# Kernel optimization log

Measured on AMD Instinct MI355X. Metric: run time of the kernel, lower is better.

The kernel has to match this reference:

```python
import jax, jax.numpy as jnp
import numpy as np

N = 50000   # num entities
R2 = 480    # num_rels * 2
D = 200     # h_dim
T = 4       # sequence_len (graph snapshots)
E = 100000  # edges per snapshot
L = 2       # rgcn layers
SLOPE = (1.0 / 8.0 + 1.0 / 3.0) / 2.0  # deterministic rrelu (eval-mode expected slope)


def setup_inputs() -> dict:
    key = jax.random.key(0)
    ks = jax.random.split(key, 13)
    s = 1.0 / np.sqrt(D)
    w = lambda k, shp, sc: jax.random.normal(k, shp, dtype=jnp.float32) * sc
    return {
        "src": jax.random.randint(ks[0], (T, E), 0, N, dtype=jnp.int32),
        "dst": jax.random.randint(ks[1], (T, E), 0, N, dtype=jnp.int32),
        "etype": jax.random.randint(ks[2], (T, E), 0, R2, dtype=jnp.int32),
        "dynamic_emb": w(ks[3], (N, D), 1.0),
        "emb_rel": w(ks[4], (R2, D), s),
        "W_ih": w(ks[5], (3 * D, 2 * D), s),
        "W_hh": w(ks[6], (3 * D, D), s),
        "b_ih": jnp.zeros((3 * D,), jnp.float32),
        "b_hh": jnp.zeros((3 * D,), jnp.float32),
        "W_neighbor": w(ks[7], (L, D, D), s),
        "W_loop": w(ks[8], (L, D, D), s),
        "time_gate_weight": w(ks[9], (D, D), s),
        "time_gate_bias": jnp.zeros((D,), jnp.float32),
    }


def _l2norm(x):
    n = jnp.linalg.norm(x, axis=-1, keepdims=True)
    return x / jnp.maximum(n, 1e-12)


def _gru(x, hprev, W_ih, W_hh, b_ih, b_hh):
    gi = x @ W_ih.T + b_ih
    gh = hprev @ W_hh.T + b_hh
    ir, iz, inn = jnp.split(gi, 3, axis=-1)
    hr, hz, hn = jnp.split(gh, 3, axis=-1)
    r = jax.nn.sigmoid(ir + hr)
    z = jax.nn.sigmoid(iz + hz)
    n = jnp.tanh(inn + r * hn)
    return (1.0 - z) * n + z * hprev


def reference(src, dst, etype, dynamic_emb, emb_rel, W_ih, W_hh, b_ih, b_hh,
              W_neighbor, W_loop, time_gate_weight, time_gate_bias):
    h_init = _l2norm(dynamic_emb)  # layer_norm=True path (F.normalize)

    def step(carry, g):
        h, h0 = carry
        s, d_, et = g
        # per-relation mean of entity embeddings touching that relation (r_to_e spans)
        ent_idx = jnp.concatenate([s, d_])          # [2E]
        seg = jnp.concatenate([et, et])             # [2E]
        ssum = jax.ops.segment_sum(h[ent_idx], seg, num_segments=R2)
        cnt = jax.ops.segment_sum(jnp.ones_like(seg, jnp.float32), seg, num_segments=R2)
        x_mean = ssum / jnp.maximum(cnt, 1.0)[:, None]          # absent rels stay 0
        x_input = jnp.concatenate([emb_rel, x_mean], axis=1)    # [R2, 2D]
        h0 = _l2norm(_gru(x_input, h0, W_ih, W_hh, b_ih, b_hh))
        # UnionRGCNLayer x L: gather -> sum-aggregate -> norm + self-loop -> rrelu
        deg = jax.ops.segment_sum(jnp.ones_like(d_, jnp.float32), d_, num_segments=N)
        norm = 1.0 / jnp.maximum(deg, 1.0)
        hh = h
        for l in range(L):
            pre = hh[s] + h0[et]                                  # [E, D]
            agg = jax.ops.segment_sum(pre, d_, num_segments=N) @ W_neighbor[l]
            out = agg * norm[:, None] + hh @ W_loop[l]
            hh = jnp.where(out >= 0, out, out * SLOPE)            # rrelu (eval)
        cur = _l2norm(hh)
        tw = jax.nn.sigmoid(h @ time_gate_weight + time_gate_bias)
        h = tw * cur + (1.0 - tw) * h
        return (h, h0), h

    (_, _), hist = jax.lax.scan(step, (h_init, emb_rel), (src, dst, etype))
    return hist  # [T, N, D] history of evolved entity embeddings
```

## Files before the change

### kernel.cpp

```cpp
#include <hip/hip_runtime.h>
#include <math.h>

#define NE 50000
#define R2C 480
#define DD 200
#define TT 4
#define EE 100000
#define SLOPE 0.22916666666666666f

#define SCCH 8
#define EPB (256 * SCCH)
#define APAD 224
#define WPAD 224
#define WSZ (208 * WPAD)
#define DCH 4096
#define DNC ((NE + DCH - 1) / DCH)

typedef short short8 __attribute__((ext_vector_type(8)));
typedef float float4v __attribute__((ext_vector_type(4)));

__device__ __forceinline__ float sigm(float x) { return 1.f / (1.f + expf(-x)); }

__device__ __forceinline__ short f2bf(float f) {
  union { float f; unsigned u; } v;
  v.f = f;
  unsigned r = v.u + 0x7fffu + ((v.u >> 16) & 1u);
  return (short)(r >> 16);
}


__global__ void init_h_kernel(const float* __restrict__ emb, float* __restrict__ h) {
  int n = blockIdx.x;
  int lane = threadIdx.x;
  size_t base = (size_t)n * DD;
  float v0 = emb[base + lane];
  float v1 = emb[base + 64 + lane];
  float v2 = emb[base + 128 + lane];
  float v3 = (lane < 8) ? emb[base + 192 + lane] : 0.f;
  float ss = v0 * v0 + v1 * v1 + v2 * v2 + v3 * v3;
#pragma unroll
  for (int off = 32; off; off >>= 1) ss += __shfl_down(ss, off);
  ss = __shfl(ss, 0);
  float inv = 1.f / fmaxf(sqrtf(ss), 1e-12f);
  h[base + lane] = v0 * inv;
  h[base + 64 + lane] = v1 * inv;
  h[base + 128 + lane] = v2 * inv;
  if (lane < 8) h[base + 192 + lane] = v3 * inv;
}

__global__ void copy_kernel(const float* __restrict__ a, float* __restrict__ b, int n) {
  int i = blockIdx.x * blockDim.x + threadIdx.x;
  if (i < n) b[i] = a[i];
}

__global__ void fill_x_kernel(const float* __restrict__ emb_rel, float* __restrict__ X) {
  int i = blockIdx.x * blockDim.x + threadIdx.x;
  if (i >= R2C * DD) return;
  int r = i / DD, d = i - r * DD;
  X[(size_t)r * 400 + d] = emb_rel[i];
}

__global__ void prep_w_kernel(const float* __restrict__ Wnb, const float* __restrict__ Wlp,
                              const float* __restrict__ Wtg, short* __restrict__ Wb) {
  int idx = blockIdx.x * 256 + threadIdx.x;
  if (idx >= 5 * WSZ) return;
  int m = idx / WSZ, rem = idx - m * WSZ;
  int n = rem / WPAD, k = rem - n * WPAD;
  const float* s;
  if (m == 0) s = Wnb;
  else if (m == 1) s = Wnb + DD * DD;
  else if (m == 2) s = Wlp;
  else if (m == 3) s = Wlp + DD * DD;
  else s = Wtg;
  float v = (n < DD && k < DD) ? s[(size_t)k * DD + n] : 0.f;
  Wb[idx] = f2bf(v);
}

__global__ __launch_bounds__(256) void hist_kernel(const int* __restrict__ et,
                                                   const int* __restrict__ dst,
                                                   int* __restrict__ et_hist,
                                                   int* __restrict__ deg_hist) {
  __shared__ int lh[R2C];
  int t = blockIdx.y;
  int tid = threadIdx.x;
  int e0 = blockIdx.x * EPB;
  for (int i = tid; i < R2C; i += 256) lh[i] = 0;
  __syncthreads();
#pragma unroll
  for (int c = 0; c < SCCH; c++) {
    int e = e0 + c * 256 + tid;
    if (e < EE) {
      atomicAdd(&lh[et[(size_t)t * EE + e]], 1);
      atomicAdd(&deg_hist[(size_t)t * NE + dst[(size_t)t * EE + e]], 1);
    }
  }
  __syncthreads();
  for (int i = tid; i < R2C; i += 256)
    if (lh[i]) atomicAdd(&et_hist[t * R2C + i], lh[i]);
}

__global__ void scan_rel_kernel(const int* __restrict__ et_hist, int* __restrict__ rowptr) {
  int t = blockIdx.x;
  int tid = threadIdx.x;
  __shared__ int s[512];
  int v = (tid < R2C) ? 2 * et_hist[t * R2C + tid] : 0;
  s[tid] = v;
  __syncthreads();
  for (int off = 1; off < 512; off <<= 1) {
    int x = (tid >= off) ? s[tid - off] : 0;
    __syncthreads();
    s[tid] += x;
    __syncthreads();
  }
  if (tid < R2C) rowptr[t * (R2C + 1) + tid] = s[tid] - v;
  if (tid == 0) rowptr[t * (R2C + 1) + R2C] = 2 * EE;
}

__global__ __launch_bounds__(256) void deg_partial_kernel(const int* __restrict__ deg_hist,
                                                          int* __restrict__ csum) {
  int t = blockIdx.y, c = blockIdx.x, tid = threadIdx.x;
  const int* dh = deg_hist + (size_t)t * NE;
  int base = c * DCH + tid * 16;
  int s = 0;
  if (base < NE) {
    int end = base + 16 > NE ? NE : base + 16;
    for (int i = base; i < end; i++) s += dh[i];
  }
  __shared__ int red[256];
  red[tid] = s;
  __syncthreads();
  for (int off = 128; off; off >>= 1) {
    if (tid < off) red[tid] += red[tid + off];
    __syncthreads();
  }
  if (tid == 0) csum[t * DNC + c] = red[0];
}

__global__ __launch_bounds__(256) void deg_emit_kernel(const int* __restrict__ deg_hist,
                                                       const int* __restrict__ csum,
                                                       int* __restrict__ rowptr,
                                                       float* __restrict__ normv) {
  int t = blockIdx.y, c = blockIdx.x, tid = threadIdx.x;
  const int* dh = deg_hist + (size_t)t * NE;
  __shared__ int scan[256];
  __shared__ int soff;
  int base = c * DCH + tid * 16;
  int s = 0;
  if (base < NE) {
    int end = base + 16 > NE ? NE : base + 16;
    for (int i = base; i < end; i++) s += dh[i];
  }
  scan[tid] = s;
  __syncthreads();
  for (int off = 1; off < 256; off <<= 1) {
    int x = (tid >= off) ? scan[tid - off] : 0;
    __syncthreads();
    scan[tid] += x;
    __syncthreads();
  }
  if (tid == 0) {
    int o = 0;
    for (int j = 0; j < c; j++) o += csum[t * DNC + j];
    soff = o;
  }
  __syncthreads();
  int run = soff + scan[tid] - s;
  if (base < NE) {
    int end = base + 16 > NE ? NE : base + 16;
    for (int i = base; i < end; i++) {
      int v = dh[i];
      rowptr[t * (NE + 1) + i] = run;
      normv[(size_t)t * NE + i] = 1.f / fmaxf((float)v, 1.f);
      run += v;
    }
  }
  if (c == 0 && tid == 0) rowptr[t * (NE + 1) + NE] = EE;
}

__global__ __launch_bounds__(256) void scatter_rel_kernel(const int* __restrict__ src,
                                                          const int* __restrict__ dst,
                                                          const int* __restrict__ et,
                                                          const int* __restrict__ rowptr,
                                                          int* __restrict__ cursor,
                                                          int* __restrict__ sorted_ent) {
  __shared__ int lcnt[R2C];
  __shared__ int lbase[R2C];
  int t = blockIdx.y;
  int tid = threadIdx.x;
  int e0 = blockIdx.x * EPB;
  for (int i = tid; i < R2C; i += 256) lcnt[i] = 0;
  __syncthreads();
  int rels[SCCH];
#pragma unroll
  for (int c = 0; c < SCCH; c++) {
    int e = e0 + c * 256 + tid;
    int r = (e < EE) ? et[(size_t)t * EE + e] : -1;
    rels[c] = r;
    if (r >= 0) atomicAdd(&lcnt[r], 2);
  }
  __syncthreads();
  const int* rp = rowptr + t * (R2C + 1);
  for (int i = tid; i < R2C; i += 256) {
    int c = lcnt[i];
    lbase[i] = rp[i] + (c ? atomicAdd(&cursor[t * R2C + i], c) : 0);
    lcnt[i] = 0;
  }
  __syncthreads();
  int* se = sorted_ent + (size_t)t * 2 * EE;
#pragma unroll
  for (int c = 0; c < SCCH; c++) {
    int r = rels[c];
    if (r >= 0) {
      int e = e0 + c * 256 + tid;
      int off = atomicAdd(&lcnt[r], 2);
      int p = lbase[r] + off;
      se[p] = src[(size_t)t * EE + e];
      se[p + 1] = dst[(size_t)t * EE + e];
    }
  }
}

__global__ void scatter_dst_kernel(const int* __restrict__ dst, const int* __restrict__ rowptr,
                                   int* __restrict__ cursor, int* __restrict__ sorted_edge) {
  int i = blockIdx.x * blockDim.x + threadIdx.x;
  if (i >= TT * EE) return;
  int t = i / EE, e = i - t * EE;
  int d = dst[i];
  int base = rowptr[t * (NE + 1) + d];
  int p = base + atomicAdd(&cursor[(size_t)t * NE + d], 1);
  sorted_edge[(size_t)t * EE + p] = e;
}


__global__ void relmean_part_kernel(const float* __restrict__ h, const int* __restrict__ rowptr,
                                    const int* __restrict__ sorted_ent_t,
                                    float* __restrict__ Xpart) {
  int r = blockIdx.x, j = blockIdx.y;
  int beg = rowptr[r], end = rowptr[r + 1];
  int lane = threadIdx.x & 63, w = threadIdx.x >> 6;
  float a0 = 0, a1 = 0, a2 = 0, a3 = 0;
  for (int i = beg + j * 4 + w; i < end; i += 16) {
    int idx = sorted_ent_t[i];
    const float* row = h + (size_t)idx * DD;
    a0 += row[lane];
    a1 += row[64 + lane];
    a2 += row[128 + lane];
    if (lane < 8) a3 += row[192 + lane];
  }
  __shared__ float part[4][DD];
  part[w][lane] = a0;
  part[w][64 + lane] = a1;
  part[w][128 + lane] = a2;
  if (lane < 8) part[w][192 + lane] = a3;
  __syncthreads();
  for (int d = threadIdx.x; d < DD; d += 256) {
    Xpart[((size_t)r * 4 + j) * DD + d] = part[0][d] + part[1][d] + part[2][d] + part[3][d];
  }
}

__global__ void relmean_comb_kernel(const float* __restrict__ Xpart,
                                    const int* __restrict__ rowptr, float* __restrict__ X) {
  int r = blockIdx.x;
  int d = threadIdx.x;
  if (d >= DD) return;
  float s = 0.f;
#pragma unroll
  for (int j = 0; j < 4; j++) s += Xpart[((size_t)r * 4 + j) * DD + d];
  float cnt = fmaxf((float)(rowptr[r + 1] - rowptr[r]), 1.f);
  X[(size_t)r * 400 + 200 + d] = s / cnt;
}

__global__ __launch_bounds__(256) void gemm_small_bt(const float* __restrict__ A,
                                                     const float* __restrict__ B,
                                                     float* __restrict__ C, int M, int N, int K) {
  __shared__ float As[16][33];
  __shared__ float Bs[16][33];
  int tid = threadIdx.x;
  int col0 = blockIdx.x * 32;
  int row0 = blockIdx.y * 32;
  int tr = tid >> 4, tc = tid & 15;
  float a00 = 0, a01 = 0, a10 = 0, a11 = 0;
  for (int k0 = 0; k0 < K; k0 += 16) {
    __syncthreads();
    for (int i = tid; i < 512; i += 256) {
      int kk = i & 15, r = i >> 4;
      int row = row0 + r, k = k0 + kk;
      As[kk][r] = (row < M && k < K) ? A[(size_t)row * K + k] : 0.f;
    }
    for (int i = tid; i < 512; i += 256) {
      int kk = i & 15, c = i >> 4;
      int col = col0 + c, k = k0 + kk;
      Bs[kk][c] = (col < N && k < K) ? B[(size_t)col * K + k] : 0.f;
    }
    __syncthreads();
#pragma unroll
    for (int kk = 0; kk < 16; kk++) {
      float x0 = As[kk][tr * 2], x1 = As[kk][tr * 2 + 1];
      float y0 = Bs[kk][tc * 2], y1 = Bs[kk][tc * 2 + 1];
      a00 += x0 * y0;
      a01 += x0 * y1;
      a10 += x1 * y0;
      a11 += x1 * y1;
    }
  }
  int row = row0 + tr * 2, col = col0 + tc * 2;
  if (row < M && col < N) C[(size_t)row * N + col] = a00;
  if (row < M && col + 1 < N) C[(size_t)row * N + col + 1] = a01;
  if (row + 1 < M && col < N) C[(size_t)(row + 1) * N + col] = a10;
  if (row + 1 < M && col + 1 < N) C[(size_t)(row + 1) * N + col + 1] = a11;
}

__global__ void gru_gate_kernel(const float* __restrict__ gi, const float* __restrict__ gh,
                                const float* __restrict__ b_ih, const float* __restrict__ b_hh,
                                float* __restrict__ h0) {
  int r = blockIdx.x;
  int tid = threadIdx.x;
  int lane = tid & 63, w = tid >> 6;
  __shared__ float red[4];
  float o = 0.f;
  if (tid < DD) {
    size_t b = (size_t)r * (3 * DD);
    float ir = gi[b + tid] + b_ih[tid];
    float iz = gi[b + DD + tid] + b_ih[DD + tid];
    float inn = gi[b + 2 * DD + tid] + b_ih[2 * DD + tid];
    float hr = gh[b + tid] + b_hh[tid];
    float hz = gh[b + DD + tid] + b_hh[DD + tid];
    float hn = gh[b + 2 * DD + tid] + b_hh[2 * DD + tid];
    float hv = h0[(size_t)r * DD + tid];
    float rr = sigm(ir + hr);
    float z = sigm(iz + hz);
    float n = tanhf(inn + rr * hn);
    o = (1.f - z) * n + z * hv;
  }
  float ss = o * o;
#pragma unroll
  for (int off = 32; off; off >>= 1) ss += __shfl_down(ss, off);
  if (lane == 0) red[w] = ss;
  __syncthreads();
  float tot = red[0] + red[1] + red[2] + red[3];
  float inv = 1.f / fmaxf(sqrtf(tot), 1e-12f);
  if (tid < DD) h0[(size_t)r * DD + tid] = o * inv;
}

__global__ void agg_kernel(const float* __restrict__ hh, const float* __restrict__ h0,
                           const int* __restrict__ rowptr, const int* __restrict__ sorted_edge_t,
                           const int* __restrict__ src_t, const int* __restrict__ et_t,
                           const float* __restrict__ normv_t, short* __restrict__ aggb) {
  int w = threadIdx.x >> 6, lane = threadIdx.x & 63;
  int n = blockIdx.x * 4 + w;
  if (n >= NE) return;
  int beg = rowptr[n], end = rowptr[n + 1];
  float a0 = 0, a1 = 0, a2 = 0, a3 = 0;
  for (int i = beg; i < end; i++) {
    int e = sorted_edge_t[i];
    const float* hr = hh + (size_t)src_t[e] * DD;
    const float* qr = h0 + (size_t)et_t[e] * DD;
    a0 += hr[lane] + qr[lane];
    a1 += hr[64 + lane] + qr[64 + lane];
    a2 += hr[128 + lane] + qr[128 + lane];
    if (lane < 8) a3 += hr[192 + lane] + qr[192 + lane];
  }
  float nm = normv_t[n];
  short* outp = aggb + (size_t)n * APAD;
  outp[lane] = f2bf(a0 * nm);
  outp[64 + lane] = f2bf(a1 * nm);
  outp[128 + lane] = f2bf(a2 * nm);
  if (lane < 8) outp[192 + lane] = f2bf(a3 * nm);
  else if (lane < 32) outp[192 + lane] = 0;
}


__global__ __launch_bounds__(256) void gemm_dual(const short* __restrict__ A1,
                                                 const short* __restrict__ Wb1,
                                                 const float* __restrict__ A2,
                                                 const short* __restrict__ Wb2,
                                                 float* __restrict__ C) {
  __shared__ short Bt[208][40];
  int tid = threadIdx.x;
  int lane = tid & 63, w = tid >> 6;
  int quad = lane >> 4, l16 = lane & 15;
  int row0 = blockIdx.x * 128;

  float4v acc[2][13];
#pragma unroll
  for (int rt = 0; rt < 2; rt++)
#pragma unroll
    for (int ct = 0; ct < 13; ct++) acc[rt][ct] = (float4v){0.f, 0.f, 0.f, 0.f};

  for (int pass = 0; pass < 2; ++pass) {
    const short* Wb = pass ? Wb2 : Wb1;
    for (int k0 = 0; k0 < DD; k0 += 32) {
      __syncthreads();
#pragma unroll
      for (int it = 0; it < 4; it++) {
        int c = tid + it * 256;
        if (c < 832) {
          int n = c % 208, k8 = (c / 208) * 8;
          *(short8*)&Bt[n][k8] = *(const short8*)&Wb[(size_t)n * WPAD + k0 + k8];
        }
      }
      __syncthreads();
      short8 af[2];
#pragma unroll
      for (int rt = 0; rt < 2; rt++) {
        int row = row0 + w * 32 + rt * 16 + l16;
        short8 a = (short8){0, 0, 0, 0, 0, 0, 0, 0};
        if (pass == 0) {
          if (row < NE) a = *(const short8*)(A1 + (size_t)row * APAD + k0 + quad * 8);
        } else {
          int kb = k0 + quad * 8;
          if (row < NE && kb < DD) {
            const float* ap = A2 + (size_t)row * DD + kb;
            float4v v0 = *(const float4v*)ap;
            float4v v1 = *(const float4v*)(ap + 4);
            short tmp[8] = {f2bf(v0[0]), f2bf(v0[1]), f2bf(v0[2]), f2bf(v0[3]),
                            f2bf(v1[0]), f2bf(v1[1]), f2bf(v1[2]), f2bf(v1[3])};
            a = *(short8*)&tmp[0];
          }
        }
        af[rt] = a;
      }
#pragma unroll
      for (int ct = 0; ct < 13; ct++) {
        short8 bf = *(short8*)&Bt[ct * 16 + l16][quad * 8];
        acc[0][ct] = __builtin_amdgcn_mfma_f32_16x16x32_bf16(af[0], bf, acc[0][ct], 0, 0, 0);
        acc[1][ct] = __builtin_amdgcn_mfma_f32_16x16x32_bf16(af[1], bf, acc[1][ct], 0, 0, 0);
      }
    }
  }
#pragma unroll
  for (int rt = 0; rt < 2; rt++) {
#pragma unroll
    for (int ct = 0; ct < 13; ct++) {
      int col = ct * 16 + l16;
      if (col >= DD) continue;
#pragma unroll
      for (int i = 0; i < 4; i++) {
        int row = row0 + w * 32 + rt * 16 + quad * 4 + i;
        if (row < NE) {
          float v = acc[rt][ct][i];
          v = (v >= 0.f) ? v : v * SLOPE;
          C[(size_t)row * DD + col] = v;
        }
      }
    }
  }
}

__global__ __launch_bounds__(256) void gemm_tgfin(const float* __restrict__ A,
                                                  const short* __restrict__ Wb,
                                                  const float* __restrict__ hh,
                                                  const float* __restrict__ tgb,
                                                  float* __restrict__ outp) {
  __shared__ short Bt[208][40];
  int tid = threadIdx.x;
  int lane = tid & 63, w = tid >> 6;
  int quad = lane >> 4, l16 = lane & 15;
  int row0 = blockIdx.x * 128;

  float4v acc[2][13];
#pragma unroll
  for (int rt = 0; rt < 2; rt++)
#pragma unroll
    for (int ct = 0; ct < 13; ct++) acc[rt][ct] = (float4v){0.f, 0.f, 0.f, 0.f};

  for (int k0 = 0; k0 < DD; k0 += 32) {
    __syncthreads();
#pragma unroll
    for (int it = 0; it < 4; it++) {
      int c = tid + it * 256;
      if (c < 832) {
        int n = c % 208, k8 = (c / 208) * 8;
        *(short8*)&Bt[n][k8] = *(const short8*)&Wb[(size_t)n * WPAD + k0 + k8];
      }
    }
    __syncthreads();
    short8 af[2];
#pragma unroll
    for (int rt = 0; rt < 2; rt++) {
      int row = row0 + w * 32 + rt * 16 + l16;
      short8 a = (short8){0, 0, 0, 0, 0, 0, 0, 0};
      int kb = k0 + quad * 8;
      if (row < NE && kb < DD) {
        const float* ap = A + (size_t)row * DD + kb;
        float4v v0 = *(const float4v*)ap;
        float4v v1 = *(const float4v*)(ap + 4);
        short tmp[8] = {f2bf(v0[0]), f2bf(v0[1]), f2bf(v0[2]), f2bf(v0[3]),
                        f2bf(v1[0]), f2bf(v1[1]), f2bf(v1[2]), f2bf(v1[3])};
        a = *(short8*)&tmp[0];
      }
      af[rt] = a;
    }
#pragma unroll
    for (int ct = 0; ct < 13; ct++) {
      short8 bf = *(short8*)&Bt[ct * 16 + l16][quad * 8];
      acc[0][ct] = __builtin_amdgcn_mfma_f32_16x16x32_bf16(af[0], bf, acc[0][ct], 0, 0, 0);
      acc[1][ct] = __builtin_amdgcn_mfma_f32_16x16x32_bf16(af[1], bf, acc[1][ct], 0, 0, 0);
    }
  }
#pragma unroll
  for (int rt = 0; rt < 2; rt++) {
#pragma unroll
    for (int i = 0; i < 4; i++) {
      int row = row0 + w * 32 + rt * 16 + quad * 4 + i;
      bool rok = row < NE;
      size_t rb = (size_t)row * DD;
      float ssq = 0.f;
#pragma unroll
      for (int ct = 0; ct < 13; ct++) {
        int col = ct * 16 + l16;
        float x = (rok && col < DD) ? hh[rb + col] : 0.f;
        ssq += x * x;
      }
#pragma unroll
      for (int off = 1; off < 16; off <<= 1) ssq += __shfl_xor(ssq, off);
      float inv = 1.f / fmaxf(sqrtf(ssq), 1e-12f);
#pragma unroll
      for (int ct = 0; ct < 13; ct++) {
        int col = ct * 16 + l16;
        if (rok && col < DD) {
          float cur = hh[rb + col] * inv;
          float tw = sigm(acc[rt][ct][i] + tgb[col]);
          outp[rb + col] = tw * cur + (1.f - tw) * A[rb + col];
        }
      }
    }
  }
}


extern "C" void kernel_launch(void* const* d_in, const int* in_sizes, int n_in, void* d_out,
                              int out_size, void* d_ws, size_t ws_size, hipStream_t stream) {
  const int* src = (const int*)d_in[0];
  const int* dst = (const int*)d_in[1];
  const int* et = (const int*)d_in[2];
  const float* dyn = (const float*)d_in[3];
  const float* emb_rel = (const float*)d_in[4];
  const float* W_ih = (const float*)d_in[5];
  const float* W_hh = (const float*)d_in[6];
  const float* b_ih = (const float*)d_in[7];
  const float* b_hh = (const float*)d_in[8];
  const float* W_nb = (const float*)d_in[9];
  const float* W_lp = (const float*)d_in[10];
  const float* Wtg = (const float*)d_in[11];
  const float* tgb = (const float*)d_in[12];
  float* out = (float*)d_out;

  char* p = (char*)d_ws;
  float* h = (float*)p;        p += (size_t)NE * DD * 4;
  float* bufB = (float*)p;     p += (size_t)NE * DD * 4;
  float* agg = (float*)p;      p += (size_t)NE * DD * 4;
  float* h0 = (float*)p;       p += (size_t)R2C * DD * 4;
  float* X = (float*)p;        p += (size_t)R2C * 400 * 4;
  float* normv = (float*)p;    p += (size_t)TT * NE * 4;
  int* et_rowptr = (int*)p;    p += (size_t)TT * (R2C + 1) * 4;
  int* et_cursor = (int*)p;    p += (size_t)TT * R2C * 4;
  int* et_hist = (int*)p;      p += (size_t)TT * R2C * 4;
  int* sorted_ent = (int*)p;   p += (size_t)TT * 2 * EE * 4;
  int* dst_rowptr = (int*)p;   p += (size_t)TT * (NE + 1) * 4;
  int* dst_cursor = (int*)p;   p += (size_t)TT * NE * 4;
  int* deg_hist = (int*)p;     p += (size_t)TT * NE * 4;
  int* sorted_edge = (int*)p;  p += (size_t)TT * EE * 4;
  short* Wb = (short*)p;       p += (size_t)5 * WSZ * 2;
  float* Xpart = (float*)p;    p += (size_t)R2C * 4 * DD * 4;
  int* csum = (int*)p;         p += (size_t)TT * DNC * 4;

  float* gi = bufB;
  float* gh = bufB + (size_t)R2C * 3 * DD;
  short* aggb = (short*)agg;

  hipMemsetAsync(et_hist, 0, (size_t)TT * R2C * 4, stream);
  hipMemsetAsync(deg_hist, 0, (size_t)TT * NE * 4, stream);
  hipMemsetAsync(et_cursor, 0, (size_t)TT * R2C * 4, stream);
  hipMemsetAsync(dst_cursor, 0, (size_t)TT * NE * 4, stream);

  init_h_kernel<<<NE, 64, 0, stream>>>(dyn, h);
  copy_kernel<<<(R2C * DD + 255) / 256, 256, 0, stream>>>(emb_rel, h0, R2C * DD);
  fill_x_kernel<<<(R2C * DD + 255) / 256, 256, 0, stream>>>(emb_rel, X);
  prep_w_kernel<<<(5 * WSZ + 255) / 256, 256, 0, stream>>>(W_nb, W_lp, Wtg, Wb);
  const dim3 bin_grid((EE + EPB - 1) / EPB, TT);
  hist_kernel<<<bin_grid, 256, 0, stream>>>(et, dst, et_hist, deg_hist);
  scan_rel_kernel<<<TT, 512, 0, stream>>>(et_hist, et_rowptr);
  const dim3 deg_grid(DNC, TT);
  deg_partial_kernel<<<deg_grid, 256, 0, stream>>>(deg_hist, csum);
  deg_emit_kernel<<<deg_grid, 256, 0, stream>>>(deg_hist, csum, dst_rowptr, normv);
  scatter_rel_kernel<<<bin_grid, 256, 0, stream>>>(src, dst, et, et_rowptr, et_cursor, sorted_ent);
  scatter_dst_kernel<<<(TT * EE + 255) / 256, 256, 0, stream>>>(dst, dst_rowptr, dst_cursor,
                                                                sorted_edge);

  const int gemm_grid = (NE + 127) / 128;
  const dim3 gru_grid((3 * DD + 31) / 32, (R2C + 31) / 32);
  const dim3 rm_grid(R2C, 4);
  for (int t = 0; t < TT; t++) {
    const int* src_t = src + (size_t)t * EE;
    const int* et_t = et + (size_t)t * EE;
    const float* hcur = (t == 0) ? h : out + (size_t)(t - 1) * NE * DD;
    float* bufA = out + (size_t)t * NE * DD;

    relmean_part_kernel<<<rm_grid, 256, 0, stream>>>(hcur, et_rowptr + t * (R2C + 1),
                                                     sorted_ent + (size_t)t * 2 * EE, Xpart);
    relmean_comb_kernel<<<R2C, 256, 0, stream>>>(Xpart, et_rowptr + t * (R2C + 1), X);
    gemm_small_bt<<<gru_grid, 256, 0, stream>>>(X, W_ih, gi, R2C, 3 * DD, 2 * DD);
    gemm_small_bt<<<gru_grid, 256, 0, stream>>>(h0, W_hh, gh, R2C, 3 * DD, DD);
    gru_gate_kernel<<<R2C, 256, 0, stream>>>(gi, gh, b_ih, b_hh, h0);
    agg_kernel<<<(NE + 3) / 4, 256, 0, stream>>>(hcur, h0, dst_rowptr + t * (NE + 1),
                                                 sorted_edge + (size_t)t * EE, src_t, et_t,
                                                 normv + (size_t)t * NE, aggb);
    gemm_dual<<<gemm_grid, 256, 0, stream>>>(aggb, Wb + 0 * WSZ, hcur, Wb + 2 * WSZ, bufA);
    agg_kernel<<<(NE + 3) / 4, 256, 0, stream>>>(bufA, h0, dst_rowptr + t * (NE + 1),
                                                 sorted_edge + (size_t)t * EE, src_t, et_t,
                                                 normv + (size_t)t * NE, aggb);
    gemm_dual<<<gemm_grid, 256, 0, stream>>>(aggb, Wb + 1 * WSZ, bufA, Wb + 3 * WSZ, bufB);
    gemm_tgfin<<<gemm_grid, 256, 0, stream>>>(hcur, Wb + 4 * WSZ, bufB, tgb, bufA);
  }
}
```

Baseline: 1.495 ms.

## Preload A fragments in registers and halve GEMM row tile to 64

The dual and time-gate GEMMs now use 64-row blocks with one 16-row tile per wave instead of two. Each wave loads its full A row fragments (all K chunks) into registers up front, so global loads are issued early and not stalled behind the LDS barriers. The dual GEMM stages both weight matrices into a double LDS buffer per K chunk, which halves the number of sync rounds. In exchange the grid doubles, so each block reuses its weight tile across fewer rows, and the extra fragment registers may lower occupancy.

```diff
diff --git a/kernel.cpp b/kernel.cpp
--- a/kernel.cpp
+++ b/kernel.cpp
@@ -375,73 +375,73 @@
                                                  const float* __restrict__ A2,
                                                  const short* __restrict__ Wb2,
                                                  float* __restrict__ C) {
-  __shared__ short Bt[208][40];
+  __shared__ short Bt[2][208][40];
   int tid = threadIdx.x;
   int lane = tid & 63, w = tid >> 6;
   int quad = lane >> 4, l16 = lane & 15;
-  int row0 = blockIdx.x * 128;
-
-  float4v acc[2][13];
-#pragma unroll
-  for (int rt = 0; rt < 2; rt++)
-#pragma unroll
-    for (int ct = 0; ct < 13; ct++) acc[rt][ct] = (float4v){0.f, 0.f, 0.f, 0.f};
-
-  for (int pass = 0; pass < 2; ++pass) {
-    const short* Wb = pass ? Wb2 : Wb1;
-    for (int k0 = 0; k0 < DD; k0 += 32) {
-      __syncthreads();
-#pragma unroll
-      for (int it = 0; it < 4; it++) {
-        int c = tid + it * 256;
-        if (c < 832) {
-          int n = c % 208, k8 = (c / 208) * 8;
-          *(short8*)&Bt[n][k8] = *(const short8*)&Wb[(size_t)n * WPAD + k0 + k8];
-        }
+  int row = blockIdx.x * 64 + w * 16 + l16;
+  bool rok = row < NE;
+
+  short8 af1[7], af2[7];
+#pragma unroll
+  for (int c = 0; c < 7; c++) {
+    af1[c] = rok ? *(const short8*)(A1 + (size_t)row * APAD + c * 32 + quad * 8)
+                 : (short8){0, 0, 0, 0, 0, 0, 0, 0};
+  }
+#pragma unroll
+  for (int c = 0; c < 7; c++) {
+    int kb = c * 32 + quad * 8;
+    short8 a = (short8){0, 0, 0, 0, 0, 0, 0, 0};
+    if (rok && kb < DD) {
+      const float* ap = A2 + (size_t)row * DD + kb;
+      float4v v0 = *(const float4v*)ap;
+      float4v v1 = *(const float4v*)(ap + 4);
+      short tmp[8] = {f2bf(v0[0]), f2bf(v0[1]), f2bf(v0[2]), f2bf(v0[3]),
+                      f2bf(v1[0]), f2bf(v1[1]), f2bf(v1[2]), f2bf(v1[3])};
+      a = *(short8*)&tmp[0];
+    }
+    af2[c] = a;
+  }
+
+  float4v acc[13];
+#pragma unroll
+  for (int ct = 0; ct < 13; ct++) acc[ct] = (float4v){0.f, 0.f, 0.f, 0.f};
+
+#pragma unroll
+  for (int c = 0; c < 7; c++) {
+    __syncthreads();
+#pragma unroll
+    for (int it = 0; it < 7; it++) {
+      int s = tid + it * 256;
+      if (s < 1664) {
+        int m = s >= 832;
+        int ss = s - m * 832;
+        int n = ss % 208, k8 = (ss / 208) * 8;
+        const short* Wb = m ? Wb2 : Wb1;
+        *(short8*)&Bt[m][n][k8] = *(const short8*)&Wb[(size_t)n * WPAD + c * 32 + k8];
       }
-      __syncthreads();
-      short8 af[2];
-#pragma unroll
-      for (int rt = 0; rt < 2; rt++) {
-        int row = row0 + w * 32 + rt * 16 + l16;
-        short8 a = (short8){0, 0, 0, 0, 0, 0, 0, 0};
-        if (pass == 0) {
-          if (row < NE) a = *(const short8*)(A1 + (size_t)row * APAD + k0 + quad * 8);
-        } else {
-          int kb = k0 + quad * 8;
-          if (row < NE && kb < DD) {
-            const float* ap = A2 + (size_t)row * DD + kb;
-            float4v v0 = *(const float4v*)ap;
-            float4v v1 = *(const float4v*)(ap + 4);
-            short tmp[8] = {f2bf(v0[0]), f2bf(v0[1]), f2bf(v0[2]), f2bf(v0[3]),
-                            f2bf(v1[0]), f2bf(v1[1]), f2bf(v1[2]), f2bf(v1[3])};
-            a = *(short8*)&tmp[0];
-          }
-        }
-        af[rt] = a;
-      }
-#pragma unroll
-      for (int ct = 0; ct < 13; ct++) {
-        short8 bf = *(short8*)&Bt[ct * 16 + l16][quad * 8];
-        acc[0][ct] = __builtin_amdgcn_mfma_f32_16x16x32_bf16(af[0], bf, acc[0][ct], 0, 0, 0);
-        acc[1][ct] = __builtin_amdgcn_mfma_f32_16x16x32_bf16(af[1], bf, acc[1][ct], 0, 0, 0);
-      }
-    }
-  }
-#pragma unroll
-  for (int rt = 0; rt < 2; rt++) {
+    }
+    __syncthreads();
 #pragma unroll
     for (int ct = 0; ct < 13; ct++) {
-      int col = ct * 16 + l16;
-      if (col >= DD) continue;
-#pragma unroll
-      for (int i = 0; i < 4; i++) {
-        int row = row0 + w * 32 + rt * 16 + quad * 4 + i;
-        if (row < NE) {
-          float v = acc[rt][ct][i];
-          v = (v >= 0.f) ? v : v * SLOPE;
-          C[(size_t)row * DD + col] = v;
-        }
+      short8 b1 = *(short8*)&Bt[0][ct * 16 + l16][quad * 8];
+      short8 b2 = *(short8*)&Bt[1][ct * 16 + l16][quad * 8];
+      acc[ct] = __builtin_amdgcn_mfma_f32_16x16x32_bf16(af1[c], b1, acc[ct], 0, 0, 0);
+      acc[ct] = __builtin_amdgcn_mfma_f32_16x16x32_bf16(af2[c], b2, acc[ct], 0, 0, 0);
+    }
+  }
+  int r0 = blockIdx.x * 64 + w * 16 + quad * 4;
+#pragma unroll
+  for (int ct = 0; ct < 13; ct++) {
+    int col = ct * 16 + l16;
+    if (col >= DD) continue;
+#pragma unroll
+    for (int i = 0; i < 4; i++) {
+      int r = r0 + i;
+      if (r < NE) {
+        float v = acc[ct][i];
+        v = (v >= 0.f) ? v : v * SLOPE;
+        C[(size_t)r * DD + col] = v;
       }
     }
   }
@@ -456,73 +456,70 @@
   int tid = threadIdx.x;
   int lane = tid & 63, w = tid >> 6;
   int quad = lane >> 4, l16 = lane & 15;
-  int row0 = blockIdx.x * 128;
-
-  float4v acc[2][13];
-#pragma unroll
-  for (int rt = 0; rt < 2; rt++)
-#pragma unroll
-    for (int ct = 0; ct < 13; ct++) acc[rt][ct] = (float4v){0.f, 0.f, 0.f, 0.f};
-
-  for (int k0 = 0; k0 < DD; k0 += 32) {
+  int row = blockIdx.x * 64 + w * 16 + l16;
+  bool rok = row < NE;
+
+  short8 af[7];
+#pragma unroll
+  for (int c = 0; c < 7; c++) {
+    int kb = c * 32 + quad * 8;
+    short8 a = (short8){0, 0, 0, 0, 0, 0, 0, 0};
+    if (rok && kb < DD) {
+      const float* ap = A + (size_t)row * DD + kb;
+      float4v v0 = *(const float4v*)ap;
+      float4v v1 = *(const float4v*)(ap + 4);
+      short tmp[8] = {f2bf(v0[0]), f2bf(v0[1]), f2bf(v0[2]), f2bf(v0[3]),
+                      f2bf(v1[0]), f2bf(v1[1]), f2bf(v1[2]), f2bf(v1[3])};
+      a = *(short8*)&tmp[0];
+    }
+    af[c] = a;
+  }
+
+  float4v acc[13];
+#pragma unroll
+  for (int ct = 0; ct < 13; ct++) acc[ct] = (float4v){0.f, 0.f, 0.f, 0.f};
+
+#pragma unroll
+  for (int c = 0; c < 7; c++) {
     __syncthreads();
 #pragma unroll
     for (int it = 0; it < 4; it++) {
-      int c = tid + it * 256;
-      if (c < 832) {
-        int n = c % 208, k8 = (c / 208) * 8;
-        *(short8*)&Bt[n][k8] = *(const short8*)&Wb[(size_t)n * WPAD + k0 + k8];
+      int s = tid + it * 256;
+      if (s < 832) {
+        int n = s % 208, k8 = (s / 208) * 8;
+        *(short8*)&Bt[n][k8] = *(const short8*)&Wb[(size_t)n * WPAD + c * 32 + k8];
       }
     }
     __syncthreads();
-    short8 af[2];
-#pragma unroll
-    for (int rt = 0; rt < 2; rt++) {
-      int row = row0 + w * 32 + rt * 16 + l16;
-      short8 a = (short8){0, 0, 0, 0, 0, 0, 0, 0};
-      int kb = k0 + quad * 8;
-      if (row < NE && kb < DD) {
-        const float* ap = A + (size_t)row * DD + kb;
-        float4v v0 = *(const float4v*)ap;
-        float4v v1 = *(const float4v*)(ap + 4);
-        short tmp[8] = {f2bf(v0[0]), f2bf(v0[1]), f2bf(v0[2]), f2bf(v0[3]),
-                        f2bf(v1[0]), f2bf(v1[1]), f2bf(v1[2]), f2bf(v1[3])};
-        a = *(short8*)&tmp[0];
-      }
-      af[rt] = a;
-    }
 #pragma unroll
     for (int ct = 0; ct < 13; ct++) {
       short8 bf = *(short8*)&Bt[ct * 16 + l16][quad * 8];
-      acc[0][ct] = __builtin_amdgcn_mfma_f32_16x16x32_bf16(af[0], bf, acc[0][ct], 0, 0, 0);
-      acc[1][ct] = __builtin_amdgcn_mfma_f32_16x16x32_bf16(af[1], bf, acc[1][ct], 0, 0, 0);
-    }
-  }
-#pragma unroll
-  for (int rt = 0; rt < 2; rt++) {
-#pragma unroll
-    for (int i = 0; i < 4; i++) {
-      int row = row0 + w * 32 + rt * 16 + quad * 4 + i;
-      bool rok = row < NE;
-      size_t rb = (size_t)row * DD;
-      float ssq = 0.f;
-#pragma unroll
-      for (int ct = 0; ct < 13; ct++) {
-        int col = ct * 16 + l16;
-        float x = (rok && col < DD) ? hh[rb + col] : 0.f;
-        ssq += x * x;
-      }
-#pragma unroll
-      for (int off = 1; off < 16; off <<= 1) ssq += __shfl_xor(ssq, off);
-      float inv = 1.f / fmaxf(sqrtf(ssq), 1e-12f);
-#pragma unroll
-      for (int ct = 0; ct < 13; ct++) {
-        int col = ct * 16 + l16;
-        if (rok && col < DD) {
-          float cur = hh[rb + col] * inv;
-          float tw = sigm(acc[rt][ct][i] + tgb[col]);
-          outp[rb + col] = tw * cur + (1.f - tw) * A[rb + col];
-        }
+      acc[ct] = __builtin_amdgcn_mfma_f32_16x16x32_bf16(af[c], bf, acc[ct], 0, 0, 0);
+    }
+  }
+  int rbase = blockIdx.x * 64 + w * 16 + quad * 4;
+#pragma unroll
+  for (int i = 0; i < 4; i++) {
+    int r = rbase + i;
+    bool ok = r < NE;
+    size_t rb = (size_t)r * DD;
+    float ssq = 0.f;
+#pragma unroll
+    for (int ct = 0; ct < 13; ct++) {
+      int col = ct * 16 + l16;
+      float x = (ok && col < DD) ? hh[rb + col] : 0.f;
+      ssq += x * x;
+    }
+#pragma unroll
+    for (int off = 1; off < 16; off <<= 1) ssq += __shfl_xor(ssq, off);
+    float inv = 1.f / fmaxf(sqrtf(ssq), 1e-12f);
+#pragma unroll
+    for (int ct = 0; ct < 13; ct++) {
+      int col = ct * 16 + l16;
+      if (ok && col < DD) {
+        float cur = hh[rb + col] * inv;
+        float tw = sigm(acc[ct][i] + tgb[col]);
+        outp[rb + col] = tw * cur + (1.f - tw) * A[rb + col];
       }
     }
   }
@@ -588,7 +585,7 @@
   scatter_dst_kernel<<<(TT * EE + 255) / 256, 256, 0, stream>>>(dst, dst_rowptr, dst_cursor,
                                                                 sorted_edge);
 
-  const int gemm_grid = (NE + 127) / 128;
+  const int gemm_grid = (NE + 63) / 64;
   const dim3 gru_grid((3 * DD + 31) / 32, (R2C + 31) / 32);
   const dim3 rm_grid(R2C, 4);
   for (int t = 0; t < TT; t++) {
```

Result: slower. 1.568 ms (+4.9%).
